# Kernel optimization log

Measured on AMD Instinct MI355X. Metric: run time of the kernel, lower is better.

Reference implementation:

```python
import jax, jax.numpy as jnp
import numpy as np

BN_EPS = 1e-5


def setup_inputs() -> dict:
    key = jax.random.key(0)
    ks = jax.random.split(key, 11)
    C, P = 256, 128  # inplanes, planes = inplanes // 2
    B, H, W = 4, 64, 64
    s = 0.01  # conv weight init std in the original module
    return {
        "x": jax.random.normal(ks[0], (B, C, H, W), jnp.float32),
        "Wt": jax.random.normal(ks[1], (P, C), jnp.float32) * s,
        "bt": jnp.zeros((P,), jnp.float32),
        "Wp": jax.random.normal(ks[2], (P, C), jnp.float32) * s,
        "bp": jnp.zeros((P,), jnp.float32),
        "Wg": jax.random.normal(ks[3], (P, C), jnp.float32) * s,
        "bg": jnp.zeros((P,), jnp.float32),
        "Wz": jax.random.normal(ks[4], (C, P), jnp.float32) * s,
        "bz": jnp.zeros((C,), jnp.float32),
        "gamma": jax.random.uniform(ks[5], (C,), jnp.float32),
        "beta": jax.random.normal(ks[6], (C,), jnp.float32) * 0.01,
    }


def reference(x, Wt, bt, Wp, bp, Wg, bg, Wz, bz, gamma, beta):
    b, c, h, w = x.shape
    n = h * w
    xf = x.reshape(b, c, n)  # (b, c, n)
    # 1x1 conv projections == per-pixel matmuls
    t = jnp.einsum("pc,bcn->bnp", Wt, xf) + bt            # (b, n, p) queries
    p = jnp.einsum("pc,bcn->bpn", Wp, xf) + bp[:, None]   # (b, p, n) keys
    g = jnp.einsum("pc,bcn->bnp", Wg, xf) + bg            # (b, n, p) values
    planes = Wt.shape[0]
    scale = jnp.asarray(planes, x.dtype) ** 0.5
    att = jnp.einsum("bnp,bpm->bnm", t, p) / scale        # (b, n, n)
    att = jax.nn.softmax(att, axis=-1)                    # softmax over dim 2
    y = jnp.einsum("bnm,bmp->bnp", att, g)                # (b, n, p)
    z = jnp.einsum("cp,bnp->bcn", Wz, y) + bz[:, None]    # (b, c, n)
    z = z.reshape(b, c, h, w)
    # BatchNorm2d, training-mode batch statistics over (B, H, W)
    mean = z.mean(axis=(0, 2, 3))
    var = z.var(axis=(0, 2, 3))
    zn = (z - mean[:, None, None]) * jax.lax.rsqrt(var + BN_EPS)[:, None, None]
    out = zn * gamma[:, None, None] + beta[:, None, None] + x
    return out
```

## Files before the change

### kernel.cpp

```cpp
#include <hip/hip_runtime.h>


#define SCALE_ 0.08838834764831845f

typedef __bf16 bf16x8 __attribute__((ext_vector_type(8)));
typedef float f32x4 __attribute__((ext_vector_type(4)));
typedef unsigned short ushort8v __attribute__((ext_vector_type(8)));

__device__ inline unsigned short f2bf(float f) {
  unsigned int u = __float_as_uint(f);
  u += 0x7fffu + ((u >> 16) & 1u);
  return (unsigned short)(u >> 16);
}
__device__ inline float bflo(unsigned int u) { return __uint_as_float(u << 16); }
__device__ inline float bfhi(unsigned int u) { return __uint_as_float(u & 0xffff0000u); }

__device__ inline void gl16(const unsigned short* g, unsigned short* l) {
  __builtin_amdgcn_global_load_lds(
      (const __attribute__((address_space(1))) unsigned int*)(g),
      (__attribute__((address_space(3))) unsigned int*)(l), 16, 0, 0);
}

__global__ __launch_bounds__(256) void prep_kernel(
    const float* __restrict__ x,
    const float* __restrict__ Wt, const float* __restrict__ Wp, const float* __restrict__ Wg,
    unsigned short* __restrict__ xT, unsigned short* __restrict__ Wb) {
  const int tid = threadIdx.x;
  const int bx = blockIdx.x, b = blockIdx.y;
  if (bx >= 64) {
    if (b != 0) return;
#pragma unroll
    for (int it = 0; it < 3; ++it) {
      int k = (bx - 64) * 256 + tid + it * 4096;
      const float* src = (k < 4096 ? Wt : (k < 8192 ? Wp : Wg)) + (size_t)(k & 4095) * 8;
      float4 a = *(const float4*)src, c = *(const float4*)(src + 4);
      ushort8v us;
      us[0] = f2bf(a.x); us[1] = f2bf(a.y); us[2] = f2bf(a.z); us[3] = f2bf(a.w);
      us[4] = f2bf(c.x); us[5] = f2bf(c.y); us[6] = f2bf(c.z); us[7] = f2bf(c.w);
      *(ushort8v*)(Wb + (size_t)k * 8) = us;
    }
    return;
  }
  __shared__ float sT[128 * 68];
  const int w = tid >> 6, l = tid & 63;
  const int n0 = bx * 64;
  for (int half = 0; half < 2; ++half) {
    if (half) __syncthreads();
#pragma unroll
    for (int it = 0; it < 8; ++it) {
      int e = it * 256 + tid;
      int c = e >> 4, n4 = e & 15;
      float4 v = *(const float4*)(x + (size_t)(b * 256 + half * 128 + c) * 4096 + n0 + n4 * 4);
      *(float4*)(sT + c * 68 + n4 * 4) = v;
    }
    __syncthreads();
#pragma unroll
    for (int it = 0; it < 4; ++it) {
      int c8 = it * 4 + w;
      int n = l;
      ushort8v us;
#pragma unroll
      for (int j = 0; j < 8; ++j) us[j] = f2bf(sT[(c8 * 8 + j) * 68 + n]);
      *(ushort8v*)(xT + (size_t)b * 1048576 + (size_t)(n0 + n) * 256 + half * 128 + c8 * 8) = us;
    }
  }
}

__global__ __launch_bounds__(256, 3) void proj_kernel(
    const unsigned short* __restrict__ xT, const unsigned short* __restrict__ Wb,
    const float* __restrict__ bt, const float* __restrict__ bp, const float* __restrict__ bg,
    unsigned short* __restrict__ Qb, unsigned short* __restrict__ Kb,
    unsigned short* __restrict__ Vtb) {
  __shared__ unsigned short sX[64 * 256];
  __shared__ unsigned short sW[128 * 64];
  const int tid = threadIdx.x;
  const int w = tid >> 6, l = tid & 63;
  const int l15 = l & 15, lh = l >> 4;
  const int n0 = blockIdx.x * 64;
  const int b = blockIdx.y;
  const int sel = blockIdx.z;
  const unsigned short* xTb = xT + (size_t)b * 1048576;
  const unsigned short* Ws = Wb + (size_t)sel * 32768;
#pragma unroll
  for (int it = 0; it < 8; ++it) {
    int row = w * 16 + it * 2 + (l >> 5);
    int s = l & 31;
    int src = (s & 24) | ((s & 7) ^ (row & 7));
    gl16(xTb + (size_t)(n0 + row) * 256 + src * 8, sX + (w * 16 + it * 2) * 256);
  }
  f32x4 acc[2][4];
#pragma unroll
  for (int mt = 0; mt < 2; ++mt)
#pragma unroll
    for (int nt = 0; nt < 4; ++nt) acc[mt][nt] = (f32x4){0.f, 0.f, 0.f, 0.f};

  for (int ko4 = 0; ko4 < 4; ++ko4) {
    __syncthreads();
#pragma unroll
    for (int it = 0; it < 4; ++it) {
      int p = w * 32 + it * 8 + (l >> 3);
      int s = l & 7;
      gl16(Ws + (size_t)p * 256 + ko4 * 64 + ((s ^ (p & 7)) * 8),
           sW + (w * 32 + it * 8) * 64);
    }
    __syncthreads();
#pragma unroll
    for (int ko2 = 0; ko2 < 2; ++ko2) {
      bf16x8 af[2];
#pragma unroll
      for (int mt = 0; mt < 2; ++mt) {
        int p = w * 32 + mt * 16 + l15;
        af[mt] = *(const bf16x8*)(sW + p * 64 + (((ko2 * 4 + lh) ^ (p & 7)) << 3));
      }
#pragma unroll
      for (int nt = 0; nt < 4; ++nt) {
        int n = nt * 16 + l15;
        int ci = ko4 * 8 + ko2 * 4 + lh;
        int slot = (ci & 24) | ((ci & 7) ^ (n & 7));
        bf16x8 bfv = *(const bf16x8*)(sX + n * 256 + (slot << 3));
#pragma unroll
        for (int mt = 0; mt < 2; ++mt)
          acc[mt][nt] = __builtin_amdgcn_mfma_f32_16x16x32_bf16(af[mt], bfv, acc[mt][nt], 0, 0, 0);
      }
    }
  }
  const float* bias = sel == 0 ? bt : (sel == 1 ? bp : bg);
  const float scl = sel == 0 ? SCALE_ : 1.0f;
#pragma unroll
  for (int mt = 0; mt < 2; ++mt) {
    int pb = w * 32 + mt * 16 + lh * 4;
    float4 bv = *(const float4*)(bias + pb);
    const float* bvf = (const float*)&bv;
    if (sel < 2) {
      unsigned short* dst = (sel == 0 ? Qb : Kb) + (size_t)b * 524288;
#pragma unroll
      for (int nt = 0; nt < 4; ++nt) {
        ushort4 us;
        us.x = f2bf((acc[mt][nt][0] + bv.x) * scl);
        us.y = f2bf((acc[mt][nt][1] + bv.y) * scl);
        us.z = f2bf((acc[mt][nt][2] + bv.z) * scl);
        us.w = f2bf((acc[mt][nt][3] + bv.w) * scl);
        *(ushort4*)(dst + (size_t)(n0 + nt * 16 + l15) * 128 + pb) = us;
      }
    } else {
      unsigned short* dst = Vtb + (size_t)b * 524288;
#pragma unroll
      for (int nt = 0; nt < 4; ++nt)
#pragma unroll
        for (int r = 0; r < 4; ++r)
          dst[(size_t)(pb + r) * 4096 + n0 + nt * 16 + l15] = f2bf(acc[mt][nt][r] + bvf[r]);
    }
  }
}

__global__ __launch_bounds__(256, 4) void attn_kernel(
    const unsigned short* __restrict__ Qb, const unsigned short* __restrict__ Kb,
    const unsigned short* __restrict__ Vtb, unsigned short* __restrict__ Ytp,
    float* __restrict__ denp) {
  __shared__ unsigned short sm[20480];
  const int tid = threadIdx.x;
  const int w = tid >> 6, l = tid & 63;
  const int l15 = l & 15, lh = l >> 4;
  const int b = blockIdx.y, sp = blockIdx.z;
  const int n0 = blockIdx.x * 64;
  const int kvbase = sp * 1024;

  bf16x8 qf[4];
  {
    const unsigned short* qrow = Qb + (size_t)(b * 4096 + n0 + w * 16 + l15) * 128 + lh * 8;
#pragma unroll
    for (int ko = 0; ko < 4; ++ko) qf[ko] = *(const bf16x8*)(qrow + ko * 32);
  }
  unsigned short* kb = sm;
  unsigned short* vb = sm + 8192;
  unsigned short* sP = sm + 16384 + w * 1024;

  f32x4 yacc[8];
#pragma unroll
  for (int i = 0; i < 8; ++i) yacc[i] = (f32x4){0.f, 0.f, 0.f, 0.f};
  float den = 0.f;

  const unsigned short* Kbase = Kb + (size_t)(b * 4096 + kvbase) * 128;
  const unsigned short* Vbase = Vtb + (size_t)(b * 128) * 4096 + kvbase;

  const int kmrow_off = l >> 4;
  const int vdrow_off = l >> 3;

  for (int t = 0; t < 16; ++t) {
    const int koff = t * 64;
    __syncthreads();
#pragma unroll
    for (int it = 0; it < 4; ++it) {
      int mrow = w * 16 + it * 4 + kmrow_off;
      gl16(Kbase + (size_t)(koff + mrow) * 128 + (((l & 15) ^ (mrow & 7)) << 3),
           kb + (w * 16 + it * 4) * 128);
      int drow = w * 32 + it * 8 + vdrow_off;
      gl16(Vbase + (size_t)drow * 4096 + koff + (((l & 7) ^ (drow & 7)) << 3),
           vb + (w * 32 + it * 8) * 64);
    }
    __syncthreads();

    f32x4 sacc[4];
#pragma unroll
    for (int mt = 0; mt < 4; ++mt) sacc[mt] = (f32x4){0.f, 0.f, 0.f, 0.f};
#pragma unroll
    for (int ko = 0; ko < 4; ++ko) {
#pragma unroll
      for (int mt = 0; mt < 4; ++mt) {
        int m = mt * 16 + l15;
        bf16x8 ak = *(const bf16x8*)(kb + m * 128 + (((lh + 4 * ko) ^ (m & 7)) << 3));
        sacc[mt] = __builtin_amdgcn_mfma_f32_16x16x32_bf16(ak, qf[ko], sacc[mt], 0, 0, 0);
      }
    }
    float rs = 0.f;
#pragma unroll
    for (int mt = 0; mt < 4; ++mt) {
      float e0 = __expf(sacc[mt][0]);
      float e1 = __expf(sacc[mt][1]);
      float e2 = __expf(sacc[mt][2]);
      float e3 = __expf(sacc[mt][3]);
      rs += (e0 + e1) + (e2 + e3);
      ushort4 us;
      us.x = f2bf(e0); us.y = f2bf(e1); us.z = f2bf(e2); us.w = f2bf(e3);
      int mblk = mt * 2 + (lh >> 1);
      *(ushort4*)(sP + l15 * 64 + ((mblk ^ (l15 & 7)) << 3) + (lh & 1) * 4) = us;
    }
    rs += __shfl_xor(rs, 16);
    rs += __shfl_xor(rs, 32);
    den += rs;
#pragma unroll
    for (int ko = 0; ko < 2; ++ko) {
      bf16x8 bp = *(const bf16x8*)(sP + l15 * 64 + (((lh + 4 * ko) ^ (l15 & 7)) << 3));
#pragma unroll
      for (int dt = 0; dt < 8; ++dt) {
        int d = dt * 16 + l15;
        bf16x8 av = *(const bf16x8*)(vb + d * 64 + (((lh + 4 * ko) ^ (d & 7)) << 3));
        yacc[dt] = __builtin_amdgcn_mfma_f32_16x16x32_bf16(av, bp, yacc[dt], 0, 0, 0);
      }
    }
  }
  unsigned short* Yt = Ytp + (size_t)(sp * 4 + b) * 524288 +
                       (size_t)(n0 + w * 16 + l15) * 128;
#pragma unroll
  for (int dt = 0; dt < 8; ++dt) {
    ushort4 us;
    us.x = f2bf(yacc[dt][0]); us.y = f2bf(yacc[dt][1]);
    us.z = f2bf(yacc[dt][2]); us.w = f2bf(yacc[dt][3]);
    *(ushort4*)(Yt + dt * 16 + lh * 4) = us;
  }
  if (lh == 0) denp[(size_t)(sp * 4 + b) * 4096 + n0 + w * 16 + l15] = den;
}

__global__ __launch_bounds__(256, 4) void zbn_kernel(
    const unsigned short* __restrict__ Ytp, const float* __restrict__ denp,
    const float* __restrict__ Wz, const float* __restrict__ bz,
    float* __restrict__ Z, float* __restrict__ S1p, float* __restrict__ S2p) {
  __shared__ unsigned short sY[64 * 128];
  __shared__ unsigned short sW[64 * 128];
  __shared__ float sDen[64];
  const int tid = threadIdx.x;
  const int w = tid >> 6, l = tid & 63;
  const int l15 = l & 15, lh = l >> 4;
  const int bx = blockIdx.x;
  const int b = blockIdx.y;
  const int n0 = bx * 64;
  const int c0 = blockIdx.z * 64;
  if (tid < 64) {
    float s = 0.f;
#pragma unroll
    for (int sp = 0; sp < 4; ++sp) s += denp[sp * 16384 + b * 4096 + n0 + tid];
    sDen[tid] = 1.0f / s;
  }
  __syncthreads();
#pragma unroll
  for (int it = 0; it < 4; ++it) {
    int e = it * 256 + tid;
    int n = e >> 4, pc = e & 15;
    size_t o = (size_t)b * 524288 + (size_t)(n0 + n) * 128 + pc * 8;
    float a0 = 0, a1 = 0, a2 = 0, a3 = 0, a4 = 0, a5 = 0, a6 = 0, a7 = 0;
#pragma unroll
    for (int sp = 0; sp < 4; ++sp) {
      uint4 v = *(const uint4*)(Ytp + (size_t)sp * 2097152 + o);
      a0 += bflo(v.x); a1 += bfhi(v.x);
      a2 += bflo(v.y); a3 += bfhi(v.y);
      a4 += bflo(v.z); a5 += bfhi(v.z);
      a6 += bflo(v.w); a7 += bfhi(v.w);
    }
    float idn = sDen[n];
    ushort8v us;
    us[0] = f2bf(a0 * idn); us[1] = f2bf(a1 * idn);
    us[2] = f2bf(a2 * idn); us[3] = f2bf(a3 * idn);
    us[4] = f2bf(a4 * idn); us[5] = f2bf(a5 * idn);
    us[6] = f2bf(a6 * idn); us[7] = f2bf(a7 * idn);
    *(ushort8v*)(sY + n * 128 + ((pc ^ (n & 7)) << 3)) = us;
  }
#pragma unroll
  for (int it = 0; it < 4; ++it) {
    int e = it * 256 + tid;
    int c = e >> 4, pc = e & 15;
    const float* wsrc = Wz + (size_t)(c0 + c) * 128 + pc * 8;
    float4 wa = *(const float4*)(wsrc);
    float4 wb = *(const float4*)(wsrc + 4);
    ushort8v us;
    us[0] = f2bf(wa.x); us[1] = f2bf(wa.y); us[2] = f2bf(wa.z); us[3] = f2bf(wa.w);
    us[4] = f2bf(wb.x); us[5] = f2bf(wb.y); us[6] = f2bf(wb.z); us[7] = f2bf(wb.w);
    *(ushort8v*)(sW + c * 128 + ((pc ^ (c & 7)) << 3)) = us;
  }
  __syncthreads();
  f32x4 acc[4];
#pragma unroll
  for (int nt = 0; nt < 4; ++nt) acc[nt] = (f32x4){0.f, 0.f, 0.f, 0.f};
  const int crow = w * 16 + l15;
#pragma unroll
  for (int ko = 0; ko < 4; ++ko) {
    bf16x8 aw = *(const bf16x8*)(sW + crow * 128 + (((lh + 4 * ko) ^ (crow & 7)) << 3));
#pragma unroll
    for (int nt = 0; nt < 4; ++nt) {
      int nrow = nt * 16 + l15;
      bf16x8 by = *(const bf16x8*)(sY + nrow * 128 + (((lh + 4 * ko) ^ (nrow & 7)) << 3));
      acc[nt] = __builtin_amdgcn_mfma_f32_16x16x32_bf16(aw, by, acc[nt], 0, 0, 0);
    }
  }
  const int cb = c0 + w * 16 + lh * 4;
  float4 bzv = *(const float4*)(bz + cb);
  const float* bzf = (const float*)&bzv;
#pragma unroll
  for (int r = 0; r < 4; ++r) {
    float s1 = 0.f, s2 = 0.f;
#pragma unroll
    for (int nt = 0; nt < 4; ++nt) {
      float z = acc[nt][r] + bzf[r];
      Z[(size_t)(b * 256 + cb + r) * 4096 + n0 + nt * 16 + l15] = z;
      s1 += z;
      s2 += z * z;
    }
#pragma unroll
    for (int m = 1; m < 16; m <<= 1) {
      s1 += __shfl_xor(s1, m);
      s2 += __shfl_xor(s2, m);
    }
    if (l15 == 0) {
      S1p[(size_t)(cb + r) * 256 + b * 64 + bx] = s1;
      S2p[(size_t)(cb + r) * 256 + b * 64 + bx] = s2;
    }
  }
}

__global__ __launch_bounds__(256) void bnfin_kernel(
    const float* __restrict__ S1p, const float* __restrict__ S2p,
    const float* __restrict__ gamma, const float* __restrict__ beta,
    float* __restrict__ Scale, float* __restrict__ Shift) {
  __shared__ float r1[4], r2[4];
  const int c = blockIdx.x, tid = threadIdx.x;
  float s1 = S1p[(size_t)c * 256 + tid];
  float s2 = S2p[(size_t)c * 256 + tid];
#pragma unroll
  for (int m = 1; m < 64; m <<= 1) {
    s1 += __shfl_xor(s1, m);
    s2 += __shfl_xor(s2, m);
  }
  if ((tid & 63) == 0) { r1[tid >> 6] = s1; r2[tid >> 6] = s2; }
  __syncthreads();
  if (tid == 0) {
    float S1t = (r1[0] + r1[1]) + (r1[2] + r1[3]);
    float S2t = (r2[0] + r2[1]) + (r2[2] + r2[3]);
    const float inv_cnt = 1.0f / 16384.0f;
    float mean = S1t * inv_cnt;
    float var = fmaxf(S2t * inv_cnt - mean * mean, 0.0f);
    float inv = rsqrtf(var + 1e-5f);
    float sc = gamma[c] * inv;
    Scale[c] = sc;
    Shift[c] = beta[c] - mean * sc;
  }
}

__global__ __launch_bounds__(256) void out_kernel(
    const float* __restrict__ Z, const float* __restrict__ x,
    const float* __restrict__ Scale, const float* __restrict__ Shift,
    float* __restrict__ out) {
  int i4 = blockIdx.x * 256 + threadIdx.x;
  int flat = i4 << 2;
  int c = (flat >> 12) & 255;
  float4 z = *(const float4*)(Z + flat);
  float4 xv = *(const float4*)(x + flat);
  float sc = Scale[c], sh = Shift[c];
  float4 o;
  o.x = z.x * sc + sh + xv.x;
  o.y = z.y * sc + sh + xv.y;
  o.z = z.z * sc + sh + xv.z;
  o.w = z.w * sc + sh + xv.w;
  *(float4*)(out + flat) = o;
}

extern "C" void kernel_launch(void* const* d_in, const int* in_sizes, int n_in,
                              void* d_out, int out_size, void* d_ws, size_t ws_size,
                              hipStream_t stream) {
  (void)in_sizes; (void)n_in; (void)out_size; (void)ws_size;
  const float* x = (const float*)d_in[0];
  const float* Wt = (const float*)d_in[1];
  const float* bt = (const float*)d_in[2];
  const float* Wp = (const float*)d_in[3];
  const float* bp = (const float*)d_in[4];
  const float* Wg = (const float*)d_in[5];
  const float* bg = (const float*)d_in[6];
  const float* Wz = (const float*)d_in[7];
  const float* bz = (const float*)d_in[8];
  const float* gamma = (const float*)d_in[9];
  const float* beta = (const float*)d_in[10];

  unsigned short* Qb = (unsigned short*)d_ws;
  unsigned short* Kb = Qb + 2097152;
  unsigned short* Vtb = Kb + 2097152;
  unsigned short* Ytp = Vtb + 2097152;
  float* denp = (float*)(Ytp + 8388608);
  float* Z = denp + 65536;
  float* Scale = Z + 4194304;
  float* Shift = Scale + 256;

  unsigned short* xT = (unsigned short*)Z;
  unsigned short* Wb = (unsigned short*)denp;
  float* S1p = (float*)Qb;
  float* S2p = S1p + 65536;

  prep_kernel<<<dim3(80, 4), 256, 0, stream>>>(x, Wt, Wp, Wg, xT, Wb);
  proj_kernel<<<dim3(64, 4, 3), 256, 0, stream>>>(xT, Wb, bt, bp, bg, Qb, Kb, Vtb);
  attn_kernel<<<dim3(64, 4, 4), 256, 0, stream>>>(Qb, Kb, Vtb, Ytp, denp);
  zbn_kernel<<<dim3(64, 4, 4), 256, 0, stream>>>(Ytp, denp, Wz, bz, Z, S1p, S2p);
  bnfin_kernel<<<256, 256, 0, stream>>>(S1p, S2p, gamma, beta, Scale, Shift);
  out_kernel<<<4096, 256, 0, stream>>>(Z, x, Scale, Shift, (float*)d_out);
}
```

Measured before the change: 96.45 us.

## Double-buffer K/V tiles in attention kernel with halved tile size and setprio

The attention loop now stages 32-key K/V tiles into two alternating LDS buffers, so the global-to-LDS load of the next tile is issued before computing on the current one, leaving a single barrier per iteration. Tile size is halved so both buffers fit in slightly less LDS, with the swizzles and P-matrix layout adjusted to the narrower tiles. s_setprio raises wave priority around the MFMA blocks to favour matrix issue. In exchange there are twice as many iterations and barriers, with fewer MFMAs each to amortise per-iteration overhead.

Result: slower. 100.7 us (+4.4%).

```diff
diff --git a/kernel.cpp b/kernel.cpp
--- a/kernel.cpp
+++ b/kernel.cpp
@@ -157,7 +157,7 @@
     const unsigned short* __restrict__ Qb, const unsigned short* __restrict__ Kb,
     const unsigned short* __restrict__ Vtb, unsigned short* __restrict__ Ytp,
     float* __restrict__ denp) {
-  __shared__ unsigned short sm[20480];
+  __shared__ unsigned short sm[18432];
   const int tid = threadIdx.x;
   const int w = tid >> 6, l = tid & 63;
   const int l15 = l & 15, lh = l >> 4;
@@ -171,9 +171,7 @@
 #pragma unroll
     for (int ko = 0; ko < 4; ++ko) qf[ko] = *(const bf16x8*)(qrow + ko * 32);
   }
-  unsigned short* kb = sm;
-  unsigned short* vb = sm + 8192;
-  unsigned short* sP = sm + 16384 + w * 1024;
+  unsigned short* sPw = sm + 16384 + w * 512;
 
   f32x4 yacc[8];
 #pragma unroll
@@ -183,38 +181,46 @@
   const unsigned short* Kbase = Kb + (size_t)(b * 4096 + kvbase) * 128;
   const unsigned short* Vbase = Vtb + (size_t)(b * 128) * 4096 + kvbase;
 
-  const int kmrow_off = l >> 4;
-  const int vdrow_off = l >> 3;
-
-  for (int t = 0; t < 16; ++t) {
-    const int koff = t * 64;
+#define STAGE(T, BUFO)                                                              \
+  {                                                                                 \
+    const int koff_ = (T) * 32;                                                     \
+    _Pragma("unroll")                                                               \
+    for (int it = 0; it < 2; ++it) {                                                \
+      int krow = w * 8 + it * 4 + (l >> 4);                                         \
+      gl16(Kbase + (size_t)(koff_ + krow) * 128 + (((l & 15) ^ (krow & 7)) << 3),   \
+           sm + (BUFO) + (w * 8 + it * 4) * 128);                                   \
+      int vrow = w * 32 + it * 16 + (l >> 2);                                       \
+      gl16(Vbase + (size_t)vrow * 4096 + koff_ + (((l & 3) ^ (vrow & 3)) << 3),     \
+           sm + 8192 + (BUFO) + (w * 32 + it * 16) * 32);                           \
+    }                                                                               \
+  }
+
+  STAGE(0, 0)
+  for (int t = 0; t < 32; ++t) {
+    const int co = (t & 1) * 4096;
+    unsigned short* kb = sm + co;
+    unsigned short* vb = sm + 8192 + co;
     __syncthreads();
-#pragma unroll
-    for (int it = 0; it < 4; ++it) {
-      int mrow = w * 16 + it * 4 + kmrow_off;
-      gl16(Kbase + (size_t)(koff + mrow) * 128 + (((l & 15) ^ (mrow & 7)) << 3),
-           kb + (w * 16 + it * 4) * 128);
-      int drow = w * 32 + it * 8 + vdrow_off;
-      gl16(Vbase + (size_t)drow * 4096 + koff + (((l & 7) ^ (drow & 7)) << 3),
-           vb + (w * 32 + it * 8) * 64);
-    }
-    __syncthreads();
-
-    f32x4 sacc[4];
-#pragma unroll
-    for (int mt = 0; mt < 4; ++mt) sacc[mt] = (f32x4){0.f, 0.f, 0.f, 0.f};
+    if (t + 1 < 32) {
+      STAGE(t + 1, co ^ 4096)
+    }
+    f32x4 sacc[2];
+#pragma unroll
+    for (int mt = 0; mt < 2; ++mt) sacc[mt] = (f32x4){0.f, 0.f, 0.f, 0.f};
+    __builtin_amdgcn_s_setprio(1);
 #pragma unroll
     for (int ko = 0; ko < 4; ++ko) {
 #pragma unroll
-      for (int mt = 0; mt < 4; ++mt) {
+      for (int mt = 0; mt < 2; ++mt) {
         int m = mt * 16 + l15;
         bf16x8 ak = *(const bf16x8*)(kb + m * 128 + (((lh + 4 * ko) ^ (m & 7)) << 3));
         sacc[mt] = __builtin_amdgcn_mfma_f32_16x16x32_bf16(ak, qf[ko], sacc[mt], 0, 0, 0);
       }
     }
+    __builtin_amdgcn_s_setprio(0);
     float rs = 0.f;
 #pragma unroll
-    for (int mt = 0; mt < 4; ++mt) {
+    for (int mt = 0; mt < 2; ++mt) {
       float e0 = __expf(sacc[mt][0]);
       float e1 = __expf(sacc[mt][1]);
       float e2 = __expf(sacc[mt][2]);
@@ -222,22 +228,21 @@
       rs += (e0 + e1) + (e2 + e3);
       ushort4 us;
       us.x = f2bf(e0); us.y = f2bf(e1); us.z = f2bf(e2); us.w = f2bf(e3);
-      int mblk = mt * 2 + (lh >> 1);
-      *(ushort4*)(sP + l15 * 64 + ((mblk ^ (l15 & 7)) << 3) + (lh & 1) * 4) = us;
+      int bk = mt * 2 + (lh >> 1);
+      *(ushort4*)(sPw + l15 * 32 + ((bk ^ (l15 & 3)) << 3) + (lh & 1) * 4) = us;
     }
     rs += __shfl_xor(rs, 16);
     rs += __shfl_xor(rs, 32);
     den += rs;
-#pragma unroll
-    for (int ko = 0; ko < 2; ++ko) {
-      bf16x8 bp = *(const bf16x8*)(sP + l15 * 64 + (((lh + 4 * ko) ^ (l15 & 7)) << 3));
-#pragma unroll
-      for (int dt = 0; dt < 8; ++dt) {
-        int d = dt * 16 + l15;
-        bf16x8 av = *(const bf16x8*)(vb + d * 64 + (((lh + 4 * ko) ^ (d & 7)) << 3));
-        yacc[dt] = __builtin_amdgcn_mfma_f32_16x16x32_bf16(av, bp, yacc[dt], 0, 0, 0);
-      }
-    }
+    bf16x8 bp = *(const bf16x8*)(sPw + l15 * 32 + ((lh ^ (l15 & 3)) << 3));
+    __builtin_amdgcn_s_setprio(1);
+#pragma unroll
+    for (int dt = 0; dt < 8; ++dt) {
+      int d = dt * 16 + l15;
+      bf16x8 av = *(const bf16x8*)(vb + d * 32 + ((lh ^ (d & 3)) << 3));
+      yacc[dt] = __builtin_amdgcn_mfma_f32_16x16x32_bf16(av, bp, yacc[dt], 0, 0, 0);
+    }
+    __builtin_amdgcn_s_setprio(0);
   }
   unsigned short* Yt = Ytp + (size_t)(sp * 4 + b) * 524288 +
                        (size_t)(n0 + w * 16 + l15) * 128;
```

## Double-buffer K tiles, read V directly from global, use exp2 softmax

Applied to the files above, without the earlier changes.

The attention kernel now prefetches the next K tile into a second LDS buffer with async global-to-LDS loads while the current tile is computed. This drops one barrier per iteration and hides load latency. V fragments are no longer staged through LDS; each wave reads them straight from global memory, relying on L2/L1 reuse. log2(e) is folded into the Q scale so the softmax can use the native exp2 and a packed bf16 convert, and s_setprio raises wave priority around the MFMA sections. The risks are higher global read traffic and latency on the uncached V path, and a waitcnt on V that may also stall on the K prefetch.

Result: slower. 170.7 us (+77.0%).

```diff
diff --git a/kernel.cpp b/kernel.cpp
--- a/kernel.cpp
+++ b/kernel.cpp
@@ -2,6 +2,7 @@
 
 
 #define SCALE_ 0.08838834764831845f
+#define SCALE2_ 0.12752740475999508f
 
 typedef __bf16 bf16x8 __attribute__((ext_vector_type(8)));
 typedef float f32x4 __attribute__((ext_vector_type(4)));
@@ -125,7 +126,7 @@
     }
   }
   const float* bias = sel == 0 ? bt : (sel == 1 ? bp : bg);
-  const float scl = sel == 0 ? SCALE_ : 1.0f;
+  const float scl = sel == 0 ? SCALE2_ : 1.0f;
 #pragma unroll
   for (int mt = 0; mt < 2; ++mt) {
     int pb = w * 32 + mt * 16 + lh * 4;
@@ -171,9 +172,7 @@
 #pragma unroll
     for (int ko = 0; ko < 4; ++ko) qf[ko] = *(const bf16x8*)(qrow + ko * 32);
   }
-  unsigned short* kb = sm;
-  unsigned short* vb = sm + 8192;
-  unsigned short* sP = sm + 16384 + w * 1024;
+  unsigned short* sPw = sm + 16384 + w * 1024;
 
   f32x4 yacc[8];
 #pragma unroll
@@ -181,28 +180,32 @@
   float den = 0.f;
 
   const unsigned short* Kbase = Kb + (size_t)(b * 4096 + kvbase) * 128;
-  const unsigned short* Vbase = Vtb + (size_t)(b * 128) * 4096 + kvbase;
-
-  const int kmrow_off = l >> 4;
-  const int vdrow_off = l >> 3;
-
+  const unsigned short* Vgl = Vtb + (size_t)b * 524288 + kvbase;
+
+#define STAGE(T, BUFO)                                                              \
+  {                                                                                 \
+    const int koff_ = (T) * 64;                                                     \
+    _Pragma("unroll")                                                               \
+    for (int it = 0; it < 4; ++it) {                                                \
+      int krow = w * 16 + it * 4 + (l >> 4);                                        \
+      gl16(Kbase + (size_t)(koff_ + krow) * 128 + (((l & 15) ^ (krow & 7)) << 3),   \
+           sm + (BUFO) + (w * 16 + it * 4) * 128);                                  \
+    }                                                                               \
+  }
+
+  STAGE(0, 0)
   for (int t = 0; t < 16; ++t) {
+    const int co = (t & 1) * 8192;
+    const unsigned short* kb = sm + co;
     const int koff = t * 64;
     __syncthreads();
-#pragma unroll
-    for (int it = 0; it < 4; ++it) {
-      int mrow = w * 16 + it * 4 + kmrow_off;
-      gl16(Kbase + (size_t)(koff + mrow) * 128 + (((l & 15) ^ (mrow & 7)) << 3),
-           kb + (w * 16 + it * 4) * 128);
-      int drow = w * 32 + it * 8 + vdrow_off;
-      gl16(Vbase + (size_t)drow * 4096 + koff + (((l & 7) ^ (drow & 7)) << 3),
-           vb + (w * 32 + it * 8) * 64);
-    }
-    __syncthreads();
-
+    if (t + 1 < 16) {
+      STAGE(t + 1, co ^ 8192)
+    }
     f32x4 sacc[4];
 #pragma unroll
     for (int mt = 0; mt < 4; ++mt) sacc[mt] = (f32x4){0.f, 0.f, 0.f, 0.f};
+    __builtin_amdgcn_s_setprio(1);
 #pragma unroll
     for (int ko = 0; ko < 4; ++ko) {
 #pragma unroll
@@ -212,32 +215,39 @@
         sacc[mt] = __builtin_amdgcn_mfma_f32_16x16x32_bf16(ak, qf[ko], sacc[mt], 0, 0, 0);
       }
     }
-    float rs = 0.f;
-#pragma unroll
-    for (int mt = 0; mt < 4; ++mt) {
-      float e0 = __expf(sacc[mt][0]);
-      float e1 = __expf(sacc[mt][1]);
-      float e2 = __expf(sacc[mt][2]);
-      float e3 = __expf(sacc[mt][3]);
-      rs += (e0 + e1) + (e2 + e3);
-      ushort4 us;
-      us.x = f2bf(e0); us.y = f2bf(e1); us.z = f2bf(e2); us.w = f2bf(e3);
-      int mblk = mt * 2 + (lh >> 1);
-      *(ushort4*)(sP + l15 * 64 + ((mblk ^ (l15 & 7)) << 3) + (lh & 1) * 4) = us;
-    }
-    rs += __shfl_xor(rs, 16);
-    rs += __shfl_xor(rs, 32);
-    den += rs;
+    __builtin_amdgcn_s_setprio(0);
+    {
+      float rs = 0.f;
+#pragma unroll
+      for (int mt = 0; mt < 4; ++mt) {
+        float e0 = __builtin_amdgcn_exp2f(sacc[mt][0]);
+        float e1 = __builtin_amdgcn_exp2f(sacc[mt][1]);
+        float e2 = __builtin_amdgcn_exp2f(sacc[mt][2]);
+        float e3 = __builtin_amdgcn_exp2f(sacc[mt][3]);
+        rs += (e0 + e1) + (e2 + e3);
+        unsigned ua, ub;
+        asm("v_cvt_pk_bf16_f32 %0, %1, %2" : "=v"(ua) : "v"(e0), "v"(e1));
+        asm("v_cvt_pk_bf16_f32 %0, %1, %2" : "=v"(ub) : "v"(e2), "v"(e3));
+        int mblk = mt * 2 + (lh >> 1);
+        uint2 uv; uv.x = ua; uv.y = ub;
+        *(uint2*)(sPw + l15 * 64 + ((mblk ^ (l15 & 7)) << 3) + (lh & 1) * 4) = uv;
+      }
+      rs += __shfl_xor(rs, 16);
+      rs += __shfl_xor(rs, 32);
+      den += rs;
+    }
+    __builtin_amdgcn_s_setprio(1);
 #pragma unroll
     for (int ko = 0; ko < 2; ++ko) {
-      bf16x8 bp = *(const bf16x8*)(sP + l15 * 64 + (((lh + 4 * ko) ^ (l15 & 7)) << 3));
+      bf16x8 bp = *(const bf16x8*)(sPw + l15 * 64 + (((lh + 4 * ko) ^ (l15 & 7)) << 3));
 #pragma unroll
       for (int dt = 0; dt < 8; ++dt) {
         int d = dt * 16 + l15;
-        bf16x8 av = *(const bf16x8*)(vb + d * 64 + (((lh + 4 * ko) ^ (d & 7)) << 3));
+        bf16x8 av = *(const bf16x8*)(Vgl + (size_t)d * 4096 + koff + ko * 32 + lh * 8);
         yacc[dt] = __builtin_amdgcn_mfma_f32_16x16x32_bf16(av, bp, yacc[dt], 0, 0, 0);
       }
     }
+    __builtin_amdgcn_s_setprio(0);
   }
   unsigned short* Yt = Ytp + (size_t)(sp * 4 + b) * 524288 +
                        (size_t)(n0 + w * 16 + l15) * 128;
```
